# Kernel optimization log

Measured on AMD Instinct MI355X. Metric: run time of the kernel, lower is better.

The kernel has to match this reference:

```python
import jax, jax.numpy as jnp
import numpy as np

K_CAND = 64
K_FINAL = 16
ALPHA = 0.5
CURV_RATIO = 0.5
EPS = 1e-8


def index_points(points, idx):
    # points: [B, N, C], idx: [B, ...] -> [B, ..., C]
    B, N, C = points.shape
    flat = idx.reshape(B, -1)
    g = jnp.take_along_axis(points, flat[..., None], axis=1)
    return g.reshape(idx.shape + (C,))


def fps(points, num_fps):
    # Furthest point sampling (matches pointnet2: starts from index 0).
    B, N, _ = points.shape
    barange = jnp.arange(B)

    def body(carry, _):
        mindist, last_idx = carry
        last_pt = points[barange, last_idx]                       # [B, 3]
        d = jnp.sum((points - last_pt[:, None, :]) ** 2, axis=-1)  # [B, N]
        mindist = jnp.minimum(mindist, d)
        next_idx = jnp.argmax(mindist, axis=1).astype(jnp.int32)
        return (mindist, next_idx), last_idx

    init = (jnp.full((B, N), 1e10, points.dtype), jnp.zeros((B,), jnp.int32))
    _, idxs = jax.lax.scan(body, init, None, length=num_fps)
    return idxs.T  # [B, num_fps]


def znorm(x):
    # per-cloud normalization over points dim, unbiased std like torch
    return (x - x.mean(axis=1, keepdims=True)) / (x.std(axis=1, ddof=1, keepdims=True) + EPS)


def reference(xyz, features, w1, b1, w2, b2, num_samples):
    B, N, _ = xyz.shape
    # --- candidate kNN via pairwise squared distances (same ordering as cdist) ---
    sq = jnp.sum(xyz * xyz, axis=-1)                               # [B, N]
    d2 = sq[:, :, None] + sq[:, None, :] - 2.0 * jnp.einsum('bnc,bmc->bnm', xyz, xyz)
    _, cand = jax.lax.top_k(-d2, K_CAND + 1)                       # smallest dists first
    cand = cand[:, :, 1:]                                          # drop self -> [B, N, 64]

    # --- learned neighbor scoring MLP on relative geometry/features ---
    nxyz = index_points(xyz, cand)                                 # [B, N, 64, 3]
    nfeat = index_points(features, cand)                           # [B, N, 64, C]
    rel_xyz = nxyz - xyz[:, :, None, :]
    rel_feat = nfeat - features[:, :, None, :]
    mlp_in = jnp.concatenate([rel_xyz, rel_feat], axis=-1)         # [B, N, 64, 3+C]
    h = jax.nn.gelu(mlp_in @ w1 + b1, approximate=False)
    scores = (h @ w2 + b2)[..., 0]                                 # [B, N, 64]
    _, top_in_cand = jax.lax.top_k(scores, K_FINAL)
    final_idx = jnp.take_along_axis(cand, top_in_cand, axis=2)     # [B, N, 16]

    # --- robust importance: curvature (3x3 SVD of cov) + feature variation ---
    n2xyz = index_points(xyz, final_idx)                           # [B, N, 16, 3]
    n2feat = index_points(features, final_idx)
    dxyz = n2xyz - xyz[:, :, None, :]
    cov = jnp.einsum('bnki,bnkj->bnij', dxyz, dxyz) / K_FINAL      # [B, N, 3, 3]
    s = jnp.linalg.svd(cov, compute_uv=False)                      # descending, [B, N, 3]
    l2, l1, l0 = s[..., 0] ** 2, s[..., 1] ** 2, s[..., 2] ** 2
    curvature = l0 / (l0 + l1 + l2 + EPS)
    dfeat = n2feat - features[:, :, None, :]
    feat_var = jnp.linalg.norm(dfeat, axis=-1).mean(axis=-1)       # [B, N]
    importance = znorm(curvature) + ALPHA * znorm(feat_var)

    # --- select curvature points, mask them, FPS for the rest ---
    num_curv = int(num_samples * CURV_RATIO)
    num_fps = num_samples - num_curv
    _, curv_idx = jax.lax.top_k(importance, num_curv)              # [B, num_curv]
    far_val = jnp.max(xyz) + 1.0
    barange = jnp.arange(B)[:, None]
    masked_xyz = xyz.at[barange, curv_idx].set(far_val)
    fps_idx = fps(masked_xyz, num_fps).astype(curv_idx.dtype)      # [B, num_fps]
    merged = jnp.concatenate([curv_idx, fps_idx], axis=1)          # [B, num_samples]
    sampled_xyz = index_points(xyz, merged)                        # [B, num_samples, 3]
    return sampled_xyz, merged


def setup_inputs() -> dict:
    key = jax.random.key(0)
    k1, k2, k3, k4 = jax.random.split(key, 4)
    B, N, C = 2, 8192, 64
    xyz = jax.random.normal(k1, (B, N, 3), jnp.float32)
    features = jax.random.normal(k2, (B, N, C), jnp.float32)
    fan_in1 = 3 + C
    w1 = jax.random.normal(k3, (fan_in1, 128), jnp.float32) / np.sqrt(fan_in1)
    b1 = jnp.zeros((128,), jnp.float32)
    w2 = jax.random.normal(k4, (128, 1), jnp.float32) / np.sqrt(128)
    b2 = jnp.zeros((1,), jnp.float32)
    return {"xyz": xyz, "features": features, "w1": w1, "b1": b1,
            "w2": w2, "b2": b2, "num_samples": 2048}
```

## Files before the change

kernel.cpp:

```cpp
#include <hip/hip_runtime.h>
#include <hip/hip_bf16.h>
#include <math.h>

#define N 8192
#define BATCH 2
#define NROWS (BATCH*N)

static __device__ __forceinline__ float fsubr(float a, float b){ return __fadd_rn(a, -b); }
static __device__ __forceinline__ unsigned okey(float f){
  unsigned u = __float_as_uint(f);
  return (u & 0x80000000u) ? ~u : (u | 0x80000000u);
}

__global__ void aux_kernel(const float* __restrict__ xyz, float* __restrict__ xs, float* __restrict__ ys,
                           float* __restrict__ zs, float* __restrict__ sq, float4* __restrict__ mxyz){
  int i = blockIdx.x*256 + threadIdx.x;
  if (i < NROWS){
    float x = xyz[i*3+0], y = xyz[i*3+1], z = xyz[i*3+2];
    xs[i]=x; ys[i]=y; zs[i]=z;
    sq[i] = __fadd_rn(__fadd_rn(__fmul_rn(x,x),__fmul_rn(y,y)),__fmul_rn(z,z));
    mxyz[i] = make_float4(x, y, z, 0.0f);
  }
}

__global__ void farval_kernel(const float* __restrict__ xyz, float* __restrict__ farval){
  __shared__ float lm[4];
  float m = -1e30f;
  for (int i = threadIdx.x; i < NROWS*3; i += 256) m = fmaxf(m, xyz[i]);
  for (int off = 32; off; off >>= 1) m = fmaxf(m, __shfl_down(m, off));
  if ((threadIdx.x & 63) == 0) lm[threadIdx.x >> 6] = m;
  __syncthreads();
  if (threadIdx.x == 0){
    float r = fmaxf(fmaxf(lm[0],lm[1]), fmaxf(lm[2],lm[3]));
    farval[0] = __fadd_rn(r, 1.0f);
  }
}

__global__ __launch_bounds__(128) void q_kernel(const float* __restrict__ xyz, const float* __restrict__ feat,
                                                const float* __restrict__ w1, float* __restrict__ Q){
  __shared__ float sx[16][3];
  __shared__ float sf[16][64];
  const int t = threadIdx.x;
  const int row0 = blockIdx.x * 16;
  for (int j = t; j < 1024; j += 128) sf[j>>6][j&63] = feat[(size_t)row0*64 + j];
  if (t < 48) sx[t/3][t%3] = xyz[(size_t)row0*3 + t];
  __syncthreads();
  float acc[16];
  #pragma unroll
  for (int r = 0; r < 16; ++r) acc[r] = 0.0f;
  for (int c = 0; c < 3; ++c){
    float wv = w1[c*128 + t];
    #pragma unroll
    for (int r = 0; r < 16; ++r) acc[r] = fmaf(sx[r][c], wv, acc[r]);
  }
  for (int c = 0; c < 64; ++c){
    float wv = w1[(3+c)*128 + t];
    #pragma unroll
    for (int r = 0; r < 16; ++r) acc[r] = fmaf(sf[r][c], wv, acc[r]);
  }
  #pragma unroll
  for (int r = 0; r < 16; ++r) Q[(size_t)(row0+r)*128 + t] = acc[r];
}

__global__ __launch_bounds__(512) void knn_kernel(const float* __restrict__ xs, const float* __restrict__ ys,
                                                  const float* __restrict__ zs, const float* __restrict__ sq,
                                                  int* __restrict__ cand){
  __shared__ unsigned fk[N];
  __shared__ unsigned hist[2048];
  __shared__ unsigned long long win[1024];
  __shared__ int scal[8];
  const int t = threadIdx.x;
  const int base_row = blockIdx.x * 32;
  const int b = base_row >> 13;
  const int n0 = base_row & (N-1);
  const int pbase = b * N;
  float px[16], py[16], pz[16], ps[16];
  #pragma unroll
  for (int j = 0; j < 16; ++j){
    int i = t + j*512;
    px[j] = xs[pbase+i]; py[j] = ys[pbase+i]; pz[j] = zs[pbase+i]; ps[j] = sq[pbase+i];
  }
  for (int r = 0; r < 32; ++r){
    const int n = n0 + r;
    const float qx = xs[pbase+n], qy = ys[pbase+n], qz = zs[pbase+n], qs = sq[pbase+n];
    #pragma unroll
    for (int j = 0; j < 4; ++j) hist[t + j*512] = 0;
    __syncthreads();
    #pragma unroll
    for (int j = 0; j < 16; ++j){
      int i = t + j*512;
      float dot = __fadd_rn(__fadd_rn(__fmul_rn(px[j],qx), __fmul_rn(py[j],qy)), __fmul_rn(pz[j],qz));
      float d2  = __fadd_rn(__fadd_rn(qs, ps[j]), -__fmul_rn(2.0f, dot));
      unsigned u = okey(d2);
      fk[i] = u;
      atomicAdd(&hist[u >> 21], 1u);
    }
    __syncthreads();
    if (t < 64){
      unsigned s = 0;
      for (int k2 = 0; k2 < 32; ++k2) s += hist[t*32 + k2];
      unsigned p = s;
      for (int off = 1; off < 64; off <<= 1){ unsigned v = (unsigned)__shfl_up((int)p, off); if (t >= off) p += v; }
      int excl = (int)(p - s);
      if (excl < 65 && (int)p >= 65){ scal[0] = t; scal[1] = excl; }
    }
    __syncthreads();
    {
      int g = scal[0];
      if (t < 32){
        unsigned s = hist[g*32 + t];
        unsigned p = s;
        for (int off = 1; off < 32; off <<= 1){ unsigned v = (unsigned)__shfl_up((int)p, off); if (t >= off) p += v; }
        int before = scal[1] + (int)(p - s);
        if (before < 65 && scal[1] + (int)p >= 65) scal[2] = g*32 + t;
      }
    }
    if (t == 0) scal[3] = 0;
    __syncthreads();
    unsigned B1 = (unsigned)scal[2];
    unsigned limit = (B1 >= 2047u) ? 0xFFFFFFFFu : ((B1+1u) << 21);
    #pragma unroll
    for (int j = 0; j < 16; ++j){
      int i = t + j*512;
      unsigned u = fk[i];
      if (u < limit){
        int p = atomicAdd(&scal[3], 1);
        if (p < 1024) win[p] = ((unsigned long long)u << 32) | (unsigned)i;
      }
    }
    __syncthreads();
    int m = scal[3]; if (m > 1024) m = 1024;
    for (int e = t; e < m; e += 512){
      unsigned long long me = win[e];
      int rk = 0;
      for (int j2 = 0; j2 < m; ++j2) rk += (win[j2] < me) ? 1 : 0;
      if (rk >= 1 && rk < 65) cand[(size_t)(pbase + n)*64 + (rk-1)] = (int)(me & 0xFFFFFFFFull);
    }
    __syncthreads();
  }
}

__global__ __launch_bounds__(256) void score_kernel(const float* __restrict__ xyz, const float* __restrict__ feat,
                                                    const float* __restrict__ Q, const float* __restrict__ b1,
                                                    const float* __restrict__ w2, const float* __restrict__ b2,
                                                    const int* __restrict__ cand,
                                                    float* __restrict__ curv, float* __restrict__ fv){
  __shared__ float4 sb14[32], sw24[32];
  __shared__ int ssel[4][16];
  __shared__ float sdx[4][16], sdy[4][16], sdz[4][16], snrm[4][16];
  const int t = threadIdx.x;
  if (t < 32) sb14[t] = ((const float4*)b1)[t];
  else if (t < 64) sw24[t-32] = ((const float4*)w2)[t-32];
  __syncthreads();
  const int w = t >> 6, lane = t & 63;
  const int row = blockIdx.x*4 + w;
  const int b = row >> 13;
  const int pbase = b * N;
  const int n = row & (N-1);
  const int ck = cand[(size_t)row*64 + lane];
  const float4* Qn4 = (const float4*)(Q + (size_t)row * 128);
  const float4* Qc4 = (const float4*)(Q + (size_t)(pbase + ck) * 128);
  const float ks = 0.70710678118654752440f;
  float acc = 0.0f;
  for (int c = 0; c < 32; ++c){
    float4 qc = Qc4[c], qn = Qn4[c], bb = sb14[c], ww = sw24[c];
    float p0 = (qc.x - qn.x) + bb.x;
    float g0 = 0.5f * p0 * (1.0f + erff(p0 * ks));
    acc += g0 * ww.x;
    float p1 = (qc.y - qn.y) + bb.y;
    float g1 = 0.5f * p1 * (1.0f + erff(p1 * ks));
    acc += g1 * ww.y;
    float p2 = (qc.z - qn.z) + bb.z;
    float g2 = 0.5f * p2 * (1.0f + erff(p2 * ks));
    acc += g2 * ww.z;
    float p3 = (qc.w - qn.w) + bb.w;
    float g3 = 0.5f * p3 * (1.0f + erff(p3 * ks));
    acc += g3 * ww.w;
  }
  float score = acc + b2[0];
  unsigned key = okey(score);
  int rk = 0;
  for (int j = 0; j < 64; ++j){
    unsigned kj = (unsigned)__shfl((int)key, j);
    rk += (kj > key || (kj == key && j < lane)) ? 1 : 0;
  }
  float cx = xyz[(size_t)(pbase+ck)*3+0], cy = xyz[(size_t)(pbase+ck)*3+1], cz = xyz[(size_t)(pbase+ck)*3+2];
  float qxv = xyz[(size_t)(pbase+n)*3+0], qyv = xyz[(size_t)(pbase+n)*3+1], qzv = xyz[(size_t)(pbase+n)*3+2];
  if (rk < 16){
    ssel[w][rk] = ck;
    sdx[w][rk] = fsubr(cx, qxv);
    sdy[w][rk] = fsubr(cy, qyv);
    sdz[w][rk] = fsubr(cz, qzv);
  }
  __syncthreads();
  if (lane < 16){
    int si = ssel[w][lane];
    const float4* fc4 = (const float4*)(feat + (size_t)(pbase+si)*64);
    const float4* fn4 = (const float4*)(feat + (size_t)(pbase+n)*64);
    double s = 0.0;
    for (int c = 0; c < 16; ++c){
      float4 a = fc4[c], bq = fn4[c];
      float d0 = fsubr(a.x, bq.x); s += (double)d0 * (double)d0;
      float d1 = fsubr(a.y, bq.y); s += (double)d1 * (double)d1;
      float d2 = fsubr(a.z, bq.z); s += (double)d2 * (double)d2;
      float d3 = fsubr(a.w, bq.w); s += (double)d3 * (double)d3;
    }
    snrm[w][lane] = sqrtf((float)s);
  }
  __syncthreads();
  if (lane == 0){
    double cxx=0, cxy=0, cxz=0, cyy=0, cyz=0, czz=0;
    for (int k2 = 0; k2 < 16; ++k2){
      double dx = (double)sdx[w][k2], dy = (double)sdy[w][k2], dz = (double)sdz[w][k2];
      cxx += dx*dx; cxy += dx*dy; cxz += dx*dz; cyy += dy*dy; cyz += dy*dz; czz += dz*dz;
    }
    float fxx = (float)(cxx/16.0), fxy = (float)(cxy/16.0), fxz = (float)(cxz/16.0);
    float fyy = (float)(cyy/16.0), fyz = (float)(cyz/16.0), fzz = (float)(czz/16.0);
    double a = fxx, bbv = fyy, c = fzz, d = fxy, e = fyz, f = fxz;
    double p1 = d*d + f*f + e*e;
    double e0, e1, e2v;
    if (p1 == 0.0){ e0 = a; e1 = bbv; e2v = c; }
    else {
      double q = (a + bbv + c) / 3.0;
      double aa = a - q, bq = bbv - q, cc = c - q;
      double p2 = aa*aa + bq*bq + cc*cc + 2.0*p1;
      double p = sqrt(p2 / 6.0);
      double inv = 1.0 / p;
      double bxx = aa*inv, byy = bq*inv, bzz = cc*inv, bxy = d*inv, bxz = f*inv, byz = e*inv;
      double detB = bxx*(byy*bzz - byz*byz) - bxy*(bxy*bzz - byz*bxz) + bxz*(bxy*byz - byy*bxz);
      double rr = 0.5 * detB;
      rr = fmin(1.0, fmax(-1.0, rr));
      double phi = acos(rr) / 3.0;
      e0 = q + 2.0*p*cos(phi);
      e2v = q + 2.0*p*cos(phi + 2.0943951023931953);
      e1 = 3.0*q - e0 - e2v;
    }
    double s0 = fabs(e0), s1 = fabs(e1), s2d = fabs(e2v), tt;
    if (s0 < s1){ tt=s0; s0=s1; s1=tt; }
    if (s1 < s2d){ tt=s1; s1=s2d; s2d=tt; }
    if (s0 < s1){ tt=s0; s0=s1; s1=tt; }
    float sv0 = (float)s0, sv1 = (float)s1, sv2 = (float)s2d;
    float l2f = __fmul_rn(sv0,sv0), l1f = __fmul_rn(sv1,sv1), l0f = __fmul_rn(sv2,sv2);
    float den = __fadd_rn(__fadd_rn(__fadd_rn(l0f, l1f), l2f), 1e-8f);
    curv[row] = l0f / den;
    double fs = 0.0;
    for (int k2 = 0; k2 < 16; ++k2) fs += (double)snrm[w][k2];
    fv[row] = (float)(fs / 16.0);
  }
}

static __device__ __forceinline__ double blk_sum(double v, double* lds, int t){
  for (int off = 32; off; off >>= 1) v += __shfl_down(v, off);
  int w = t >> 6, lane = t & 63;
  if (lane == 0) lds[w] = v;
  __syncthreads();
  double r = (t < 16) ? lds[t] : 0.0;
  if (t < 64){ for (int off = 8; off; off >>= 1) r += __shfl_down(r, off); }
  if (t == 0) lds[0] = r;
  __syncthreads();
  double out = lds[0];
  __syncthreads();
  return out;
}

__global__ __launch_bounds__(1024) void stats_kernel(const float* __restrict__ curv, const float* __restrict__ fv,
                                                     float* __restrict__ imp){
  __shared__ double lds[16];
  const int t = threadIdx.x;
  const int base = blockIdx.x * N;
  double sc = 0, sf = 0;
  for (int j = 0; j < 8; ++j){ int i = t + j*1024; sc += (double)curv[base+i]; sf += (double)fv[base+i]; }
  double Sc = blk_sum(sc, lds, t);
  double Sf = blk_sum(sf, lds, t);
  double mc = Sc/8192.0, mf = Sf/8192.0;
  double vc = 0, vf = 0;
  for (int j = 0; j < 8; ++j){ int i = t + j*1024;
    double d1 = (double)curv[base+i] - mc; vc += d1*d1;
    double d2 = (double)fv[base+i]  - mf; vf += d2*d2; }
  double Vc = blk_sum(vc, lds, t);
  double Vf = blk_sum(vf, lds, t);
  float mcf = (float)mc, mff = (float)mf;
  float dc = __fadd_rn((float)sqrt(Vc/8191.0), 1e-8f);
  float df = __fadd_rn((float)sqrt(Vf/8191.0), 1e-8f);
  for (int j = 0; j < 8; ++j){ int i = t + j*1024;
    float zc = fsubr(curv[base+i], mcf) / dc;
    float zf = fsubr(fv[base+i],  mff) / df;
    imp[base+i] = __fadd_rn(zc, __fmul_rn(0.5f, zf));
  }
}

__global__ __launch_bounds__(1024) void topk_kernel(const float* __restrict__ imp, int* __restrict__ merged,
                                                    float4* __restrict__ mxyz, const float* __restrict__ farval){
  __shared__ unsigned dk[N];
  __shared__ unsigned hist[2048];
  __shared__ unsigned long long win[2048];
  __shared__ int scal[8];
  const int t = threadIdx.x;
  const int b = blockIdx.x;
  const int base = b * N;
  #pragma unroll
  for (int j = 0; j < 2; ++j) hist[t + j*1024] = 0;
  if (t == 0) scal[3] = 0;
  __syncthreads();
  for (int j = 0; j < 8; ++j){
    int i = t + j*1024;
    unsigned u = ~okey(imp[base+i]);
    dk[i] = u;
    atomicAdd(&hist[u >> 21], 1u);
  }
  __syncthreads();
  if (t < 64){
    unsigned s = 0;
    for (int k2 = 0; k2 < 32; ++k2) s += hist[t*32 + k2];
    unsigned p = s;
    for (int off = 1; off < 64; off <<= 1){ unsigned v = (unsigned)__shfl_up((int)p, off); if (t >= off) p += v; }
    int excl = (int)(p - s);
    if (excl < 1024 && (int)p >= 1024){ scal[0] = t; scal[1] = excl; }
  }
  __syncthreads();
  {
    int g = scal[0];
    if (t < 32){
      unsigned s = hist[g*32 + t];
      unsigned p = s;
      for (int off = 1; off < 32; off <<= 1){ unsigned v = (unsigned)__shfl_up((int)p, off); if (t >= off) p += v; }
      int before = scal[1] + (int)(p - s);
      if (before < 1024 && scal[1] + (int)p >= 1024) scal[2] = g*32 + t;
    }
  }
  __syncthreads();
  unsigned B1 = (unsigned)scal[2];
  unsigned limit = (B1 >= 2047u) ? 0xFFFFFFFFu : ((B1+1u) << 21);
  for (int j = 0; j < 8; ++j){
    int i = t + j*1024;
    unsigned u = dk[i];
    if (u < limit){
      int p = atomicAdd(&scal[3], 1);
      if (p < 2048) win[p] = ((unsigned long long)u << 13) | (unsigned)i;
    }
  }
  __syncthreads();
  int m = scal[3]; if (m > 2048) m = 2048;
  const float far = farval[0];
  for (int e = t; e < m; e += 1024){
    unsigned long long me = win[e];
    int rk = 0;
    for (int j2 = 0; j2 < m; ++j2) rk += (win[j2] < me) ? 1 : 0;
    if (rk < 1024){
      int idx = (int)(me & 0x1FFFull);
      merged[b*2048 + rk] = idx;
      mxyz[base + idx] = make_float4(far, far, far, 0.0f);
    }
  }
}

#define DPP_MAX64(CTRL) { \
    int nlo = __builtin_amdgcn_update_dpp(0, klo, (CTRL), 0xf, 0xf, true); \
    int nhi = __builtin_amdgcn_update_dpp(0, khi, (CTRL), 0xf, 0xf, true); \
    unsigned long long nk = ((unsigned long long)(unsigned)nhi << 32) | (unsigned)nlo; \
    unsigned long long ck = ((unsigned long long)(unsigned)khi << 32) | (unsigned)klo; \
    if (nk > ck){ klo = nlo; khi = nhi; } \
  }

__global__ __launch_bounds__(256, 1) void fps_kernel(const float4* __restrict__ mxyz, int* __restrict__ merged){
  __shared__ unsigned long long slotK[3];
  const int t = threadIdx.x;
  const int b = blockIdx.x;
  const int base = b * N;
  float px[32], py[32], pz[32], md[32];
  #pragma unroll
  for (int j = 0; j < 32; ++j){
    float4 p = mxyz[base + t + j*256];
    px[j] = p.x; py[j] = p.y; pz[j] = p.z; md[j] = 1e10f;
  }
  if (t == 0){
    merged[b*2048 + 1024] = 0;
    slotK[0] = 0ull; slotK[1] = 0ull; slotK[2] = 0ull;
  }
  float4 w0 = mxyz[base];
  float lx = w0.x, ly = w0.y, lz = w0.z;
  __syncthreads();
  for (int it = 0; it < 1023; ++it){
    float bestv = -1.0f; unsigned blow = 0u;
    #pragma unroll
    for (int j = 0; j < 32; ++j){
      float dx = fsubr(px[j], lx), dy = fsubr(py[j], ly), dz = fsubr(pz[j], lz);
      float d = __fadd_rn(__fadd_rn(__fmul_rn(dx,dx), __fmul_rn(dy,dy)), __fmul_rn(dz,dz));
      float nm = fminf(md[j], d);
      md[j] = nm;
      if (nm > bestv){ bestv = nm; blow = 8191u - (unsigned)(t + (j<<8)); }
    }
    unsigned long long key = ((unsigned long long)__float_as_uint(bestv) << 13) | (unsigned long long)blow;
    int klo = (int)(unsigned)(key & 0xFFFFFFFFull);
    int khi = (int)(unsigned)(key >> 32);
    DPP_MAX64(0x111)
    DPP_MAX64(0x112)
    DPP_MAX64(0x114)
    DPP_MAX64(0x118)
    DPP_MAX64(0x142)
    DPP_MAX64(0x143)
    unsigned rlo = (unsigned)__builtin_amdgcn_readlane(klo, 63);
    unsigned rhi = (unsigned)__builtin_amdgcn_readlane(khi, 63);
    unsigned long long wkey = ((unsigned long long)rhi << 32) | rlo;
    const int s = it % 3;
    const int snext = (s == 2) ? 0 : s + 1;
    if ((t & 63) == 0) atomicMax(&slotK[s], wkey);
    if (t == 0) slotK[snext] = 0ull;
    __syncthreads();
    const unsigned long long k = slotK[s];
    const int idx = 8191 - (int)(k & 0x1FFFull);
    if (t == 0) merged[b*2048 + 1024 + it + 1] = idx;
    float4 wv = mxyz[base + idx];
    lx = wv.x; ly = wv.y; lz = wv.z;
  }
}

__global__ void finalize_kernel(const float* __restrict__ xyz, const int* __restrict__ merged,
                                float* __restrict__ out){
  int i = blockIdx.x*256 + threadIdx.x;
  if (i < BATCH*2048){
    int b = i >> 11;
    int idx = merged[i];
    out[12288 + i] = (float)idx;
    const float* p = xyz + (size_t)(b*N + idx)*3;
    out[i*3+0] = p[0]; out[i*3+1] = p[1]; out[i*3+2] = p[2];
  }
}

extern "C" void kernel_launch(void* const* d_in, const int* in_sizes, int n_in,
                              void* d_out, int out_size, void* d_ws, size_t ws_size,
                              hipStream_t stream){
  const float* xyz  = (const float*)d_in[0];
  const float* feat = (const float*)d_in[1];
  const float* w1   = (const float*)d_in[2];
  const float* b1   = (const float*)d_in[3];
  const float* w2   = (const float*)d_in[4];
  const float* b2   = (const float*)d_in[5];
  float* out = (float*)d_out;
  char* ws = (char*)d_ws;
  float*  Q      = (float*) (ws);
  int*    cand   = (int*)   (ws + 8388608);
  float*  xs     = (float*) (ws + 12582912);
  float*  ysv    = (float*) (ws + 12648448);
  float*  zsv    = (float*) (ws + 12713984);
  float*  sq     = (float*) (ws + 12779520);
  float*  curv   = (float*) (ws + 12845056);
  float*  fv     = (float*) (ws + 12910592);
  float*  imp    = (float*) (ws + 12976128);
  int*    merged = (int*)   (ws + 13041664);
  float*  farval = (float*) (ws + 13058048);
  float4* mxyz   = (float4*)(ws + 13058112);

  aux_kernel<<<64, 256, 0, stream>>>(xyz, xs, ysv, zsv, sq, mxyz);
  farval_kernel<<<1, 256, 0, stream>>>(xyz, farval);
  q_kernel<<<1024, 128, 0, stream>>>(xyz, feat, w1, Q);
  knn_kernel<<<512, 512, 0, stream>>>(xs, ysv, zsv, sq, cand);
  score_kernel<<<4096, 256, 0, stream>>>(xyz, feat, Q, b1, w2, b2, cand, curv, fv);
  stats_kernel<<<2, 1024, 0, stream>>>(curv, fv, imp);
  topk_kernel<<<2, 1024, 0, stream>>>(imp, merged, mxyz, farval);
  fps_kernel<<<2, 256, 0, stream>>>(mxyz, merged);
  finalize_kernel<<<16, 256, 0, stream>>>(xyz, merged, out);
}
```

Measured before the change: 2.006 ms.

## Restructure FPS kernel: 512 threads, LDS point table, double-buffered wave-key reduction

The FPS kernel now runs 512 threads per block with 16 points per thread instead of 256 threads with 32, which halves the serial distance loop per iteration. All points are staged in a 128KB dynamic LDS table, so the per-iteration lookup of the chosen point reads LDS rather than global memory. The shared-memory atomicMax over three rotating slots is replaced by per-wave keys written to a double-buffered array, and every thread takes the max of the 8 entries after one barrier. The trade-off is more waves joining each barrier, plus the large LDS allocation and the launch_bounds change.

```diff
diff --git a/kernel.cpp b/kernel.cpp
--- a/kernel.cpp
+++ b/kernel.cpp
@@ -362,33 +362,33 @@
     if (nk > ck){ klo = nlo; khi = nhi; } \
   }
 
-__global__ __launch_bounds__(256, 1) void fps_kernel(const float4* __restrict__ mxyz, int* __restrict__ merged){
-  __shared__ unsigned long long slotK[3];
+__global__ __launch_bounds__(512, 2) void fps_kernel(const float4* __restrict__ mxyz, int* __restrict__ merged){
+  extern __shared__ float4 stab[];
+  __shared__ unsigned long long wkey[2][8];
   const int t = threadIdx.x;
   const int b = blockIdx.x;
   const int base = b * N;
-  float px[32], py[32], pz[32], md[32];
+  float px[16], py[16], pz[16], md[16];
   #pragma unroll
-  for (int j = 0; j < 32; ++j){
-    float4 p = mxyz[base + t + j*256];
+  for (int j = 0; j < 16; ++j){
+    int i = t + j*512;
+    float4 p = mxyz[base + i];
     px[j] = p.x; py[j] = p.y; pz[j] = p.z; md[j] = 1e10f;
-  }
-  if (t == 0){
-    merged[b*2048 + 1024] = 0;
-    slotK[0] = 0ull; slotK[1] = 0ull; slotK[2] = 0ull;
-  }
-  float4 w0 = mxyz[base];
+    stab[i] = p;
+  }
+  if (t == 0) merged[b*2048 + 1024] = 0;
+  __syncthreads();
+  float4 w0 = stab[0];
   float lx = w0.x, ly = w0.y, lz = w0.z;
-  __syncthreads();
   for (int it = 0; it < 1023; ++it){
     float bestv = -1.0f; unsigned blow = 0u;
     #pragma unroll
-    for (int j = 0; j < 32; ++j){
+    for (int j = 0; j < 16; ++j){
       float dx = fsubr(px[j], lx), dy = fsubr(py[j], ly), dz = fsubr(pz[j], lz);
       float d = __fadd_rn(__fadd_rn(__fmul_rn(dx,dx), __fmul_rn(dy,dy)), __fmul_rn(dz,dz));
       float nm = fminf(md[j], d);
       md[j] = nm;
-      if (nm > bestv){ bestv = nm; blow = 8191u - (unsigned)(t + (j<<8)); }
+      if (nm > bestv){ bestv = nm; blow = 8191u - (unsigned)(t + (j<<9)); }
     }
     unsigned long long key = ((unsigned long long)__float_as_uint(bestv) << 13) | (unsigned long long)blow;
     int klo = (int)(unsigned)(key & 0xFFFFFFFFull);
@@ -399,18 +399,16 @@
     DPP_MAX64(0x118)
     DPP_MAX64(0x142)
     DPP_MAX64(0x143)
-    unsigned rlo = (unsigned)__builtin_amdgcn_readlane(klo, 63);
-    unsigned rhi = (unsigned)__builtin_amdgcn_readlane(khi, 63);
-    unsigned long long wkey = ((unsigned long long)rhi << 32) | rlo;
-    const int s = it % 3;
-    const int snext = (s == 2) ? 0 : s + 1;
-    if ((t & 63) == 0) atomicMax(&slotK[s], wkey);
-    if (t == 0) slotK[snext] = 0ull;
-    __syncthreads();
-    const unsigned long long k = slotK[s];
+    if ((t & 63) == 63)
+      wkey[it & 1][t >> 6] = ((unsigned long long)(unsigned)khi << 32) | (unsigned)klo;
+    __syncthreads();
+    const unsigned long long* wk = wkey[it & 1];
+    unsigned long long k = wk[0];
+    #pragma unroll
+    for (int i2 = 1; i2 < 8; ++i2){ unsigned long long o = wk[i2]; if (o > k) k = o; }
     const int idx = 8191 - (int)(k & 0x1FFFull);
     if (t == 0) merged[b*2048 + 1024 + it + 1] = idx;
-    float4 wv = mxyz[base + idx];
+    float4 wv = stab[idx];
     lx = wv.x; ly = wv.y; lz = wv.z;
   }
 }
@@ -458,6 +456,6 @@
   score_kernel<<<4096, 256, 0, stream>>>(xyz, feat, Q, b1, w2, b2, cand, curv, fv);
   stats_kernel<<<2, 1024, 0, stream>>>(curv, fv, imp);
   topk_kernel<<<2, 1024, 0, stream>>>(imp, merged, mxyz, farval);
-  fps_kernel<<<2, 256, 0, stream>>>(mxyz, merged);
+  fps_kernel<<<2, 512, 131072, stream>>>(mxyz, merged);
   finalize_kernel<<<16, 256, 0, stream>>>(xyz, merged, out);
 }
```

Measured after the change: 1.699 ms. 15.3% less time.
